# Performance work log

Hardware: AMD Instinct MI355X
Metric: run time of the kernel (lower is better)

Reference implementation:

```python
import jax, jax.numpy as jnp
import numpy as np


def conv2d(x, w, b):
    # x: [B,C,H,W], w: [O,C,K,K] (VALID, stride 1)
    out = jax.lax.conv_general_dilated(
        x, w, window_strides=(1, 1), padding='VALID',
        dimension_numbers=('NCHW', 'OIHW', 'NCHW'))
    return out + b[None, :, None, None]


def deform_conv2d(x, offset, w, b):
    # torchvision DeformConv2d semantics, offset_groups=1, stride=1, padding=0.
    # x: [B,C,H,W]; offset: [B, 2*K*K, Ho, Wo] with (dy, dx) interleaved per tap.
    B, C, H, W = x.shape
    O, _, K, _ = w.shape
    KK = K * K
    Ho, Wo = H - K + 1, W - K + 1
    off = offset.reshape(B, KK, 2, Ho, Wo)
    ky = (jnp.arange(KK) // K).astype(x.dtype)
    kx = (jnp.arange(KK) % K).astype(x.dtype)
    # sampling positions p0 + p_k + dp  -> [B, KK, Ho, Wo]
    py = ky[None, :, None, None] + jnp.arange(Ho, dtype=x.dtype)[None, None, :, None] + off[:, :, 0]
    px = kx[None, :, None, None] + jnp.arange(Wo, dtype=x.dtype)[None, None, None, :] + off[:, :, 1]
    y0 = jnp.floor(py)
    x0 = jnp.floor(px)
    wy = py - y0  # fractional parts
    wx = px - x0
    y0i = y0.astype(jnp.int32)
    x0i = x0.astype(jnp.int32)

    def corner(yi, xi):
        valid = ((yi >= 0) & (yi < H) & (xi >= 0) & (xi < W)).astype(x.dtype)
        yc = jnp.clip(yi, 0, H - 1)
        xc = jnp.clip(xi, 0, W - 1)
        # per-batch gather over all channels -> [B, C, KK, Ho, Wo]
        g = jax.vmap(lambda im, a, bb: im[:, a, bb])(x, yc, xc)
        return g * valid[:, None]

    v00 = corner(y0i, x0i)
    v01 = corner(y0i, x0i + 1)
    v10 = corner(y0i + 1, x0i)
    v11 = corner(y0i + 1, x0i + 1)
    wy_ = wy[:, None]  # [B,1,KK,Ho,Wo]
    wx_ = wx[:, None]
    samp = (v00 * (1 - wy_) * (1 - wx_) + v01 * (1 - wy_) * wx_
            + v10 * wy_ * (1 - wx_) + v11 * wy_ * wx_)
    out = jnp.einsum('bckhw,ock->bohw', samp, w.reshape(O, C, KK))
    return out + b[None, :, None, None]


_STAGES = [
    # (in_ch, out_ch, K)
    (1, 16, 3), (16, 32, 3), (32, 16, 5), (16, 16, 7), (16, 8, 5), (8, 4, 3),
]


def setup_inputs() -> dict:
    key = jax.random.key(0)
    keys = iter(jax.random.split(key, 64))
    inp = {'x': jax.random.normal(next(keys), (512, 1, 33, 33), dtype=jnp.float32)}
    for i, (ci, co, k) in enumerate(_STAGES, start=1):
        # offset-predicting conv: small init so offsets stay near the regular grid
        inp[f'ow{i}'] = jax.random.normal(next(keys), (2 * k * k, ci, k, k), dtype=jnp.float32) * 0.05
        inp[f'ob{i}'] = jax.random.normal(next(keys), (2 * k * k,), dtype=jnp.float32) * 0.05
        scale = 1.0 / np.sqrt(ci * k * k)
        inp[f'w{i}'] = jax.random.normal(next(keys), (co, ci, k, k), dtype=jnp.float32) * scale
        inp[f'b{i}'] = jax.random.normal(next(keys), (co,), dtype=jnp.float32) * scale
    inp['fc1_w'] = jax.random.normal(next(keys), (256, 13 * 13 * 4), dtype=jnp.float32) * (1.0 / np.sqrt(676))
    inp['fc1_b'] = jnp.zeros((256,), dtype=jnp.float32)
    inp['fc2_w'] = jax.random.normal(next(keys), (10, 256), dtype=jnp.float32) * (1.0 / np.sqrt(256))
    inp['fc2_b'] = jnp.zeros((10,), dtype=jnp.float32)
    return inp


def reference(x, ow1, ob1, w1, b1, ow2, ob2, w2, b2, ow3, ob3, w3, b3,
              ow4, ob4, w4, b4, ow5, ob5, w5, b5, ow6, ob6, w6, b6,
              fc1_w, fc1_b, fc2_w, fc2_b):
    h = jax.nn.relu(deform_conv2d(x, conv2d(x, ow1, ob1), w1, b1))
    h = jax.nn.relu(deform_conv2d(h, conv2d(h, ow2, ob2), w2, b2))
    h = deform_conv2d(h, conv2d(h, ow3, ob3), w3, b3)  # NOTE: no ReLU on stage 3 (matches source)
    h = jax.nn.relu(deform_conv2d(h, conv2d(h, ow4, ob4), w4, b4))
    h = jax.nn.relu(deform_conv2d(h, conv2d(h, ow5, ob5), w5, b5))
    h = jax.nn.relu(deform_conv2d(h, conv2d(h, ow6, ob6), w6, b6))
    flat = h.reshape(h.shape[0], -1)  # [B, 4*13*13]
    z = jax.nn.relu(flat @ fc1_w.T + fc1_b)
    return z @ fc2_w.T + fc2_b
```

## Files before the change

kernel.cpp:

```cpp
#include <hip/hip_runtime.h>

typedef __attribute__((ext_vector_type(8))) short bf16x8;
typedef __attribute__((ext_vector_type(4))) float f32x4;
typedef unsigned short ushort_t;

__device__ inline ushort_t bf16_trunc(float f) { return (ushort_t)(__float_as_uint(f) >> 16); }
__device__ inline float bf16_to_f(ushort_t u) { return __uint_as_float(((unsigned int)u) << 16); }

template<int CI, int KK, int KKPAD, int NPAD, int OC>
__global__ __launch_bounds__(256)
void wprep(const float* __restrict__ w, ushort_t* __restrict__ bhi, ushort_t* __restrict__ blo)
{
    const int idx = blockIdx.x * 256 + threadIdx.x;
    if (idx >= KKPAD * NPAD * CI) return;
    const int kk  = idx / (NPAD * CI);
    const int rem = idx - kk * (NPAD * CI);
    const int n   = rem / CI;
    const int ci  = rem - n * CI;
    const float v = (kk < KK && n < OC) ? w[((size_t)n * CI + ci) * KK + kk] : 0.f;
    const ushort_t h = bf16_trunc(v);
    bhi[idx] = h;
    blo[idx] = bf16_trunc(v - bf16_to_f(h));
}

template<int CI, int KK, int TPAD, int NPAD, int OC>
__global__ __launch_bounds__(256)
void wprep_d(const float* __restrict__ w, ushort_t* __restrict__ bhi, ushort_t* __restrict__ blo)
{
    constexpr int NPASS = (CI + 7) / 8;
    constexpr int TOTAL = NPASS * TPAD * NPAD * 8;
    const int idx = blockIdx.x * 256 + threadIdx.x;
    if (idx >= TOTAL) return;
    const int j     = idx & 7;
    const int n     = (idx >> 3) % NPAD;
    const int kslot = (idx >> 3) / NPAD;
    const int pass  = kslot / TPAD;
    const int tap   = kslot - pass * TPAD;
    const int ci    = pass * 8 + j;
    const float v = (tap < KK && n < OC && ci < CI) ? w[((size_t)n * CI + ci) * KK + tap] : 0.f;
    const ushort_t h = bf16_trunc(v);
    bhi[idx] = h;
    blo[idx] = bf16_trunc(v - bf16_to_f(h));
}

template<int CI, int K, int H, int W, int Ho, int Wo, int OC, int NTTOT, int NT0, int KSTEPS>
__global__ __launch_bounds__(256)
void conv_mfma(const ushort_t* __restrict__ Xhi, const ushort_t* __restrict__ Xlo,
               const ushort_t* __restrict__ Bhi, const ushort_t* __restrict__ Blo,
               const float* __restrict__ bias, float* __restrict__ out, int Mtotal)
{
    constexpr int NPAD = NTTOT * 16;
    constexpr int HW   = H * W;
    constexpr int HoWo = Ho * Wo;
    constexpr int NPASS = CI / 8;
    constexpr int TKS  = 32 / CI;
    constexpr int ROWS = TKS * NT0 * 16;
    constexpr int BSTR = CI + 8;
    constexpr int CH8  = CI / 8;
    constexpr int CHUNKS = ROWS * CH8;

    __shared__ __align__(16) ushort_t sBh[2][ROWS * BSTR];
    __shared__ __align__(16) ushort_t sBl[2][ROWS * BSTR];

    const int tid  = threadIdx.x;
    const int lane = tid & 63;
    const int wid  = tid >> 6;
    const int col  = lane & 15;
    const int quad = lane >> 4;

    const int mBase  = blockIdx.x * 256 + wid * 64;
    const int ntBase = blockIdx.y * NT0;

    int aBase[4];
#pragma unroll
    for (int mt = 0; mt < 4; ++mt) {
        int mm = mBase + mt * 16 + col;
        if (mm >= Mtotal) mm = Mtotal - 1;
        const int b   = mm / HoWo;
        const int pos = mm - b * HoWo;
        const int oy  = pos / Wo;
        const int ox  = pos - oy * Wo;
        aBase[mt] = b * NPASS * HW + oy * W + ox;
    }

    f32x4 acc[4][NT0];
#pragma unroll
    for (int mt = 0; mt < 4; ++mt)
#pragma unroll
        for (int nt = 0; nt < NT0; ++nt) acc[mt][nt] = (f32x4){0.f, 0.f, 0.f, 0.f};

    auto loadSlab = [&](int ks, int buf) {
        const int tap0 = ks * TKS;
        for (int i = tid; i < CHUNKS; i += 256) {
            const int row = i / CH8;
            const int c8  = i - row * CH8;
            const int t   = row / (NT0 * 16);
            const int nn  = row - t * (NT0 * 16);
            int n = ntBase * 16 + nn;
            if (n > NPAD - 1) n = NPAD - 1;
            const int g = ((tap0 + t) * NPAD + n) * CI + c8 * 8;
            *(bf16x8*)(sBh[buf] + row * BSTR + c8 * 8) = *(const bf16x8*)(Bhi + g);
            *(bf16x8*)(sBl[buf] + row * BSTR + c8 * 8) = *(const bf16x8*)(Blo + g);
        }
    };

    loadSlab(0, 0);
    __syncthreads();

#pragma unroll
    for (int ks = 0; ks < KSTEPS; ++ks) {
        if (ks + 1 < KSTEPS) loadSlab(ks + 1, (ks + 1) & 1);

        const int k0   = ks * 32 + quad * 8;
        const int tap  = k0 / CI;
        const int tloc = tap - ks * TKS;
        const int ci   = k0 - tap * CI;
        const int g    = ci >> 3;
        const int dkk  = (tap / K) * W + (tap - (tap / K) * K);

        bf16x8 ah[4], al[4];
#pragma unroll
        for (int mt = 0; mt < 4; ++mt) {
            const size_t aoff = (size_t)(aBase[mt] + g * HW + dkk) * 8;
            ah[mt] = *(const bf16x8*)(Xhi + aoff);
            al[mt] = *(const bf16x8*)(Xlo + aoff);
        }
        const ushort_t* __restrict__ bhp = sBh[ks & 1];
        const ushort_t* __restrict__ blp = sBl[ks & 1];
#pragma unroll
        for (int nt = 0; nt < NT0; ++nt) {
            const int ntg = ntBase + nt;
            if (ntg < NTTOT) {
                const int lrow = ((tloc * NT0 + nt) * 16 + col) * BSTR + ci;
                const bf16x8 bh = *(const bf16x8*)(bhp + lrow);
                const bf16x8 bl = *(const bf16x8*)(blp + lrow);
#pragma unroll
                for (int mt = 0; mt < 4; ++mt) {
                    acc[mt][nt] = __builtin_amdgcn_mfma_f32_16x16x32_bf16(ah[mt], bh, acc[mt][nt], 0, 0, 0);
                    acc[mt][nt] = __builtin_amdgcn_mfma_f32_16x16x32_bf16(al[mt], bh, acc[mt][nt], 0, 0, 0);
                    acc[mt][nt] = __builtin_amdgcn_mfma_f32_16x16x32_bf16(ah[mt], bl, acc[mt][nt], 0, 0, 0);
                }
            }
        }
        __syncthreads();
    }

#pragma unroll
    for (int mt = 0; mt < 4; ++mt) {
#pragma unroll
        for (int nt = 0; nt < NT0; ++nt) {
            const int ntg = ntBase + nt;
            const int n   = ntg * 16 + col;
            if (ntg < NTTOT && n < OC) {
                const float bv = bias[n];
#pragma unroll
                for (int r = 0; r < 4; ++r) {
                    const int m = mBase + mt * 16 + quad * 4 + r;
                    if (m < Mtotal) {
                        const int b   = m / HoWo;
                        const int pos = m - b * HoWo;
                        out[((size_t)b * OC + n) * HoWo + pos] = acc[mt][nt][r] + bv;
                    }
                }
            }
        }
    }
}

template<int K, int CI, int CO, int H, int W, int Ho, int Wo, bool RELU,
         int MT, int TPAD, bool OUTPL>
__global__ __launch_bounds__(MT * 64)
void deform_mfma(const ushort_t* __restrict__ Xhi, const ushort_t* __restrict__ Xlo,
                 const float* __restrict__ off,
                 const ushort_t* __restrict__ Bph, const ushort_t* __restrict__ Bpl,
                 const float* __restrict__ bias,
                 float* __restrict__ outF, ushort_t* __restrict__ oHi, ushort_t* __restrict__ oLo)
{
    constexpr int KK     = K * K;
    constexpr int HW     = H * W;
    constexpr int HoWo   = Ho * Wo;
    constexpr int NPASS  = CI / 8;
    constexpr int NPO    = CO / 8;
    constexpr int NT     = (CO + 15) / 16;
    constexpr int NPAD   = NT * 16;
    constexpr int STRIDE = 12;
    constexpr int nMB    = (HoWo + MT * 16 - 1) / (MT * 16);
    constexpr int THREADS = MT * 64;
    __shared__ __align__(16) float tile[HW * STRIDE];

    const int b    = blockIdx.x / nMB;
    const int mb   = blockIdx.x - b * nMB;
    const int tid  = threadIdx.x;
    const int wid  = tid >> 6;
    const int lane = tid & 63;
    const int col  = lane & 15;
    const int quad = lane >> 4;

    const int pixel0 = (mb * MT + wid) * 16;
    const int s      = pixel0 + col;
    const bool am    = (s < HoWo);
    const int oy = s / Wo, ox = s - oy * Wo;

    const float* offB = off + (size_t)b * 2 * KK * HoWo;

    f32x4 acc[NT];
#pragma unroll
    for (int nt = 0; nt < NT; ++nt) acc[nt] = (f32x4){0.f, 0.f, 0.f, 0.f};

    for (int pass = 0; pass < NPASS; ++pass) {
        __syncthreads();
        for (int pos = tid; pos < HW; pos += THREADS) {
            const size_t g = ((size_t)(b * NPASS + pass) * HW + pos) * 8;
            const bf16x8 h8 = *(const bf16x8*)(Xhi + g);
            const bf16x8 l8 = *(const bf16x8*)(Xlo + g);
#pragma unroll
            for (int c = 0; c < 8; ++c)
                tile[pos * STRIDE + c] = bf16_to_f((ushort_t)h8[c]) + bf16_to_f((ushort_t)l8[c]);
        }
        __syncthreads();

#pragma unroll
        for (int tg = 0; tg < TPAD / 4; ++tg) {
            const int tap = tg * 4 + quad;
            bf16x8 ahi = (bf16x8){0,0,0,0,0,0,0,0};
            bf16x8 alo = (bf16x8){0,0,0,0,0,0,0,0};

            if (am && tap < KK) {
                const float dy = offB[(size_t)(2 * tap + 0) * HoWo + s];
                const float dx = offB[(size_t)(2 * tap + 1) * HoWo + s];
                const float py = (float)(tap / K + oy) + dy;
                const float px = (float)(tap % K + ox) + dx;
                const float y0f = floorf(py), x0f = floorf(px);
                const float wy = py - y0f, wx = px - x0f;
                const int y0 = (int)y0f, x0 = (int)x0f;
                const int y1 = y0 + 1,   x1 = x0 + 1;

                const float m00 = (y0 >= 0 && y0 < H && x0 >= 0 && x0 < W) ? 1.f : 0.f;
                const float m01 = (y0 >= 0 && y0 < H && x1 >= 0 && x1 < W) ? 1.f : 0.f;
                const float m10 = (y1 >= 0 && y1 < H && x0 >= 0 && x0 < W) ? 1.f : 0.f;
                const float m11 = (y1 >= 0 && y1 < H && x1 >= 0 && x1 < W) ? 1.f : 0.f;

                const float w00 = (1.f - wy) * (1.f - wx) * m00;
                const float w01 = (1.f - wy) * wx         * m01;
                const float w10 = wy         * (1.f - wx) * m10;
                const float w11 = wy         * wx         * m11;

                const int y0c = min(max(y0, 0), H - 1), y1c = min(max(y1, 0), H - 1);
                const int x0c = min(max(x0, 0), W - 1), x1c = min(max(x1, 0), W - 1);
                const int i00 = (y0c * W + x0c) * STRIDE;
                const int i01 = (y0c * W + x1c) * STRIDE;
                const int i10 = (y1c * W + x0c) * STRIDE;
                const int i11 = (y1c * W + x1c) * STRIDE;

                float v00[8], v01[8], v10[8], v11[8];
                *(f32x4*)(v00) = *(const f32x4*)(tile + i00); *(f32x4*)(v00 + 4) = *(const f32x4*)(tile + i00 + 4);
                *(f32x4*)(v01) = *(const f32x4*)(tile + i01); *(f32x4*)(v01 + 4) = *(const f32x4*)(tile + i01 + 4);
                *(f32x4*)(v10) = *(const f32x4*)(tile + i10); *(f32x4*)(v10 + 4) = *(const f32x4*)(tile + i10 + 4);
                *(f32x4*)(v11) = *(const f32x4*)(tile + i11); *(f32x4*)(v11 + 4) = *(const f32x4*)(tile + i11 + 4);
#pragma unroll
                for (int j = 0; j < 8; ++j) {
                    const float sv = fmaf(v11[j], w11, fmaf(v10[j], w10,
                                     fmaf(v01[j], w01, v00[j] * w00)));
                    const ushort_t h = bf16_trunc(sv);
                    ahi[j] = (short)h;
                    alo[j] = (short)bf16_trunc(sv - bf16_to_f(h));
                }
            }

            const size_t kslot = (size_t)(pass * TPAD + tap);
#pragma unroll
            for (int nt = 0; nt < NT; ++nt) {
                const bf16x8 bh = *(const bf16x8*)(Bph + (kslot * NPAD + nt * 16 + col) * 8);
                const bf16x8 bl = *(const bf16x8*)(Bpl + (kslot * NPAD + nt * 16 + col) * 8);
                acc[nt] = __builtin_amdgcn_mfma_f32_16x16x32_bf16(ahi, bh, acc[nt], 0, 0, 0);
                acc[nt] = __builtin_amdgcn_mfma_f32_16x16x32_bf16(alo, bh, acc[nt], 0, 0, 0);
                acc[nt] = __builtin_amdgcn_mfma_f32_16x16x32_bf16(ahi, bl, acc[nt], 0, 0, 0);
            }
        }
    }

#pragma unroll
    for (int nt = 0; nt < NT; ++nt) {
        const int n = nt * 16 + col;
        if (n < CO) {
            const float bv = bias[n];
#pragma unroll
            for (int r = 0; r < 4; ++r) {
                const int m = pixel0 + quad * 4 + r;
                if (m < HoWo) {
                    float v = acc[nt][r] + bv;
                    if (RELU) v = fmaxf(v, 0.f);
                    if (OUTPL) {
                        const size_t o = (((size_t)b * NPO + (n >> 3)) * HoWo + m) * 8 + (n & 7);
                        const ushort_t h = bf16_trunc(v);
                        oHi[o] = h;
                        oLo[o] = bf16_trunc(v - bf16_to_f(h));
                    } else {
                        outF[((size_t)b * CO + n) * HoWo + m] = v;
                    }
                }
            }
        }
    }
}

template<int K, int CI, int CO, int H, int W, int Ho, int Wo, bool RELU,
         int CSPLIT, int STRIDE, int THREADS, int SPLIT, bool OUTPL>
__global__ __launch_bounds__(THREADS)
void deform_lds(const float* __restrict__ x, const float* __restrict__ off,
                const float* __restrict__ w, const float* __restrict__ bias,
                float* __restrict__ outF, ushort_t* __restrict__ oHi, ushort_t* __restrict__ oLo)
{
    constexpr int KK    = K * K;
    constexpr int HW    = H * W;
    constexpr int HoWo  = Ho * Wo;
    constexpr int NPASS = CI / CSPLIT;
    constexpr int NPO   = (CO + 7) / 8;
    constexpr int CHUNK = (HoWo + SPLIT - 1) / SPLIT;
    static_assert(CHUNK <= THREADS, "chunk must fit in one block");
    __shared__ __align__(16) float tile[HW * STRIDE];

    const int b   = blockIdx.x / SPLIT;
    const int sp  = blockIdx.x - b * SPLIT;
    const int tid = threadIdx.x;
    const int s   = sp * CHUNK + tid;
    const bool active = (tid < CHUNK) && (s < HoWo);

    const int oy = s / Wo, ox = s - oy * Wo;
    const float* offp = off + ((size_t)b * 2 * KK) * HoWo + s;

    float acc[CO];
#pragma unroll
    for (int o = 0; o < CO; ++o) acc[o] = 0.f;

    for (int pass = 0; pass < NPASS; ++pass) {
        const int cbase = pass * CSPLIT;
        __syncthreads();
        for (int pos = tid; pos < HW; pos += THREADS) {
#pragma unroll
            for (int c = 0; c < CSPLIT; ++c)
                tile[pos * STRIDE + c] = x[((size_t)b * CI + (cbase + c)) * HW + pos];
        }
        __syncthreads();

        if (active) {
            for (int kk = 0; kk < KK; ++kk) {
                const float dy = offp[(size_t)(2 * kk + 0) * HoWo];
                const float dx = offp[(size_t)(2 * kk + 1) * HoWo];
                const float py = (float)(kk / K + oy) + dy;
                const float px = (float)(kk % K + ox) + dx;
                const float y0f = floorf(py), x0f = floorf(px);
                const float wy = py - y0f, wx = px - x0f;
                const int y0 = (int)y0f, x0 = (int)x0f;
                const int y1 = y0 + 1,   x1 = x0 + 1;

                const float m00 = (y0 >= 0 && y0 < H && x0 >= 0 && x0 < W) ? 1.f : 0.f;
                const float m01 = (y0 >= 0 && y0 < H && x1 >= 0 && x1 < W) ? 1.f : 0.f;
                const float m10 = (y1 >= 0 && y1 < H && x0 >= 0 && x0 < W) ? 1.f : 0.f;
                const float m11 = (y1 >= 0 && y1 < H && x1 >= 0 && x1 < W) ? 1.f : 0.f;

                const float w00 = (1.f - wy) * (1.f - wx) * m00;
                const float w01 = (1.f - wy) * wx         * m01;
                const float w10 = wy         * (1.f - wx) * m10;
                const float w11 = wy         * wx         * m11;

                const int y0c = min(max(y0, 0), H - 1), y1c = min(max(y1, 0), H - 1);
                const int x0c = min(max(x0, 0), W - 1), x1c = min(max(x1, 0), W - 1);
                const int i00 = (y0c * W + x0c) * STRIDE;
                const int i01 = (y0c * W + x1c) * STRIDE;
                const int i10 = (y1c * W + x0c) * STRIDE;
                const int i11 = (y1c * W + x1c) * STRIDE;

                if constexpr (CSPLIT % 4 == 0) {
#pragma unroll
                    for (int cg = 0; cg < CSPLIT; cg += 4) {
                        const f32x4 v00 = *(const f32x4*)(tile + i00 + cg);
                        const f32x4 v01 = *(const f32x4*)(tile + i01 + cg);
                        const f32x4 v10 = *(const f32x4*)(tile + i10 + cg);
                        const f32x4 v11 = *(const f32x4*)(tile + i11 + cg);
#pragma unroll
                        for (int j = 0; j < 4; ++j) {
                            const float sv = fmaf(v11[j], w11, fmaf(v10[j], w10,
                                             fmaf(v01[j], w01, v00[j] * w00)));
#pragma unroll
                            for (int o = 0; o < CO; ++o)
                                acc[o] = fmaf(sv, w[(size_t)(o * CI + cbase + cg + j) * KK + kk], acc[o]);
                        }
                    }
                } else {
                    const float sv = fmaf(tile[i11], w11, fmaf(tile[i10], w10,
                                     fmaf(tile[i01], w01, tile[i00] * w00)));
#pragma unroll
                    for (int o = 0; o < CO; ++o)
                        acc[o] = fmaf(sv, w[(size_t)(o * CI + cbase) * KK + kk], acc[o]);
                }
            }
        }
    }

    if (active) {
#pragma unroll
        for (int o = 0; o < CO; ++o) {
            float v = acc[o] + bias[o];
            if (RELU) v = fmaxf(v, 0.f);
            if (OUTPL) {
                const size_t oi = (((size_t)b * NPO + (o >> 3)) * HoWo + s) * 8 + (o & 7);
                const ushort_t h = bf16_trunc(v);
                oHi[oi] = h;
                oLo[oi] = bf16_trunc(v - bf16_to_f(h));
            } else {
                outF[((size_t)b * CO + o) * HoWo + s] = v;
            }
        }
    }
}

template<int K, int CI, int NOC, int OC, int H, int W, int Ho, int Wo, int PIX>
__global__ __launch_bounds__(256)
void conv_tile(const float* __restrict__ x, const float* __restrict__ w,
               const float* __restrict__ bias, float* __restrict__ out)
{
    constexpr int KK   = K * K;
    constexpr int HoWo = Ho * Wo;
    constexpr int WoG  = (Wo + PIX - 1) / PIX;
    constexpr int G    = Ho * WoG;
    constexpr int XV   = PIX + K - 1;

    const int oc0   = blockIdx.y * NOC;
    const int g_all = blockIdx.x * 256 + threadIdx.x;
    const int b     = g_all / G;
    const int g     = g_all - b * G;
    const int oy    = g / WoG;
    const int ox0   = (g - oy * WoG) * PIX;

    const float* xbp = x + (b * CI) * (H * W) + oy * W + ox0;
    const float* wp  = w + oc0 * (CI * KK);

    float acc[PIX][NOC];
#pragma unroll
    for (int p = 0; p < PIX; ++p)
#pragma unroll
        for (int j = 0; j < NOC; ++j) acc[p][j] = bias[oc0 + j];

    const int lim = W - 1 - ox0;

    for (int ci = 0; ci < CI; ++ci) {
        const float* xc = xbp + ci * (H * W);
#pragma unroll
        for (int ky = 0; ky < K; ++ky) {
            float xv[XV];
#pragma unroll
            for (int i = 0; i < XV; ++i) {
                const int off = (i <= lim) ? i : lim;
                xv[i] = xc[ky * W + off];
            }
#pragma unroll
            for (int kx = 0; kx < K; ++kx) {
#pragma unroll
                for (int p = 0; p < PIX; ++p) {
                    const float v = xv[p + kx];
#pragma unroll
                    for (int j = 0; j < NOC; ++j)
                        acc[p][j] = fmaf(v, wp[j * (CI * KK) + ci * KK + ky * K + kx], acc[p][j]);
                }
            }
        }
    }

    float* op = out + (b * OC + oc0) * HoWo + oy * Wo + ox0;
#pragma unroll
    for (int p = 0; p < PIX; ++p) {
        if (ox0 + p < Wo) {
#pragma unroll
            for (int j = 0; j < NOC; ++j) op[j * HoWo + p] = acc[p][j];
        }
    }
}

template<int IN, int OUT>
__global__ __launch_bounds__(256)
void wtrans(const float* __restrict__ w, float* __restrict__ wt)
{
    const int idx = blockIdx.x * 256 + threadIdx.x;
    if (idx >= IN * OUT) return;
    const int i = idx / OUT, j = idx - i * OUT;
    wt[idx] = w[(size_t)j * IN + i];
}

template<int IN, int OUT, bool RELU>
__global__ __launch_bounds__(256)
void fc_t(const float* __restrict__ h, const float* __restrict__ wt,
          const float* __restrict__ bias, float* __restrict__ out, int B)
{
    const int idx = blockIdx.x * 256 + threadIdx.x;
    if (idx >= B * OUT) return;
    const int b = idx / OUT;
    const int j = idx - b * OUT;
    const float* hb = h + (size_t)b * IN;
    float acc = bias[j];
#pragma unroll 4
    for (int i = 0; i < IN; ++i)
        acc = fmaf(hb[i], wt[(size_t)i * OUT + j], acc);
    if (RELU) acc = fmaxf(acc, 0.f);
    out[idx] = acc;
}

extern "C" void kernel_launch(void* const* d_in, const int* in_sizes, int n_in,
                              void* d_out, int out_size, void* d_ws, size_t ws_size,
                              hipStream_t stream)
{
    const int B = 512;
    const float* x = (const float*)d_in[0];
    const float *ow[6], *ob[6], *w[6], *bi[6];
    for (int i = 0; i < 6; ++i) {
        ow[i] = (const float*)d_in[1 + 4 * i];
        ob[i] = (const float*)d_in[2 + 4 * i];
        w[i]  = (const float*)d_in[3 + 4 * i];
        bi[i] = (const float*)d_in[4 + 4 * i];
    }
    const float* fc1w = (const float*)d_in[25];
    const float* fc1b = (const float*)d_in[26];
    const float* fc2w = (const float*)d_in[27];
    const float* fc2b = (const float*)d_in[28];
    float* out = (float*)d_out;

    float* P   = (float*)d_ws;
    float* Q   = P  + 14000000;
    float* OFF = Q  + 14000000;
    float* Z   = OFF + 18200000;
    ushort_t* WBhi = (ushort_t*)(Z + 200000);
    ushort_t* WBlo = WBhi + 200000;
    ushort_t* WDhi = WBlo + 200000;
    ushort_t* WDlo = WDhi + 200000;
    float* WT1 = (float*)(WDlo + 200000);
    float* WT2 = WT1 + 173056;

    const dim3 blk(256);
    #define GRIDT(Ho, Wo, PIX, NG) dim3((B * (Ho) * (((Wo) + (PIX) - 1) / (PIX)) + 255) / 256, (NG), 1)
    #define CEILDIV(a, b) (((a) + (b) - 1) / (b))

    ushort_t* PL2h = (ushort_t*)Q;  ushort_t* PL2l = PL2h + (size_t)(B * 961 + 2048) * 16;
    ushort_t* PL3h = (ushort_t*)P;  ushort_t* PL3l = PL3h + (size_t)(B * 841 + 2048) * 32;
    ushort_t* PL4h = (ushort_t*)Q;  ushort_t* PL4l = PL4h + (size_t)(B * 625 + 2048) * 16;
    ushort_t* PL5h = (ushort_t*)P;  ushort_t* PL5l = PL5h + (size_t)(B * 361 + 2048) * 16;

    conv_tile<3, 1, 6, 18, 33, 33, 31, 31, 4><<<GRIDT(31, 31, 4, 3), blk, 0, stream>>>(x, ow[0], ob[0], OFF);
    deform_lds<3, 1, 16, 33, 33, 31, 31, true, 1, 1, 512, 2, true><<<dim3(B * 2), dim3(512), 0, stream>>>(x, OFF, w[0], bi[0], nullptr, PL2h, PL2l);

    {
        const int Mv = B * 841;
        wprep<16, 9, 10, 32, 18><<<CEILDIV(10 * 32 * 16, 256), blk, 0, stream>>>(ow[1], WBhi, WBlo);
        conv_mfma<16, 3, 31, 31, 29, 29, 18, 2, 2, 5><<<dim3(CEILDIV(Mv, 256), 1), blk, 0, stream>>>(PL2h, PL2l, WBhi, WBlo, ob[1], OFF, Mv);
        wprep_d<16, 9, 12, 32, 32><<<CEILDIV(2 * 12 * 32 * 8, 256), blk, 0, stream>>>(w[1], WDhi, WDlo);
        deform_mfma<3, 16, 32, 31, 31, 29, 29, true, 8, 12, true><<<dim3(B * 7), dim3(512), 0, stream>>>(PL2h, PL2l, OFF, WDhi, WDlo, bi[1], nullptr, PL3h, PL3l);
    }
    {
        const int Mv = B * 625;
        wprep<32, 25, 25, 64, 50><<<CEILDIV(25 * 64 * 32, 256), blk, 0, stream>>>(ow[2], WBhi, WBlo);
        conv_mfma<32, 5, 29, 29, 25, 25, 50, 4, 4, 25><<<dim3(CEILDIV(Mv, 256), 1), blk, 0, stream>>>(PL3h, PL3l, WBhi, WBlo, ob[2], OFF, Mv);
        wprep_d<32, 25, 28, 16, 16><<<CEILDIV(4 * 28 * 16 * 8, 256), blk, 0, stream>>>(w[2], WDhi, WDlo);
        deform_mfma<5, 32, 16, 29, 29, 25, 25, false, 8, 28, true><<<dim3(B * 5), dim3(512), 0, stream>>>(PL3h, PL3l, OFF, WDhi, WDlo, bi[2], nullptr, PL4h, PL4l);
    }
    {
        const int Mv = B * 361;
        wprep<16, 49, 50, 112, 98><<<CEILDIV(50 * 112 * 16, 256), blk, 0, stream>>>(ow[3], WBhi, WBlo);
        conv_mfma<16, 7, 25, 25, 19, 19, 98, 7, 4, 25><<<dim3(CEILDIV(Mv, 256), 2), blk, 0, stream>>>(PL4h, PL4l, WBhi, WBlo, ob[3], OFF, Mv);
        wprep_d<16, 49, 52, 16, 16><<<CEILDIV(2 * 52 * 16 * 8, 256), blk, 0, stream>>>(w[3], WDhi, WDlo);
        deform_mfma<7, 16, 16, 25, 25, 19, 19, true, 8, 52, true><<<dim3(B * 3), dim3(512), 0, stream>>>(PL4h, PL4l, OFF, WDhi, WDlo, bi[3], nullptr, PL5h, PL5l);
    }
    {
        const int Mv = B * 225;
        wprep<16, 25, 26, 64, 50><<<CEILDIV(26 * 64 * 16, 256), blk, 0, stream>>>(ow[4], WBhi, WBlo);
        conv_mfma<16, 5, 19, 19, 15, 15, 50, 4, 4, 13><<<dim3(CEILDIV(Mv, 256), 1), blk, 0, stream>>>(PL5h, PL5l, WBhi, WBlo, ob[4], OFF, Mv);
        wprep_d<16, 25, 28, 16, 8><<<CEILDIV(2 * 28 * 16 * 8, 256), blk, 0, stream>>>(w[4], WDhi, WDlo);
        deform_mfma<5, 16, 8, 19, 19, 15, 15, true, 4, 28, false><<<dim3(B * 4), dim3(256), 0, stream>>>(PL5h, PL5l, OFF, WDhi, WDlo, bi[4], Q, nullptr, nullptr);
    }
    conv_tile<3, 8, 6, 18, 15, 15, 13, 13, 4><<<GRIDT(13, 13, 4, 3), blk, 0, stream>>>(Q, ow[5], ob[5], OFF);
    deform_lds<3, 8, 4, 15, 15, 13, 13, true, 8, 12, 192, 1, false><<<dim3(B), dim3(192), 0, stream>>>(Q, OFF, w[5], bi[5], P, nullptr, nullptr);

    wtrans<676, 256><<<CEILDIV(676 * 256, 256), blk, 0, stream>>>(fc1w, WT1);
    wtrans<256, 10><<<CEILDIV(256 * 10, 256), blk, 0, stream>>>(fc2w, WT2);
    fc_t<676, 256, true><<<dim3(CEILDIV(B * 256, 256)), blk, 0, stream>>>(P, WT1, fc1b, Z, B);
    fc_t<256, 10, false><<<dim3(CEILDIV(B * 10, 256)), blk, 0, stream>>>(Z, WT2, fc2b, out, B);

    #undef GRIDT
    #undef CEILDIV
}
```

Before: 902.4 us.

## Stage 16 channels per pass and reuse bilinear weights across passes

The deformable-conv MFMA kernel now stages 16 channels per LDS pass instead of 8, which halves the number of barrier-separated passes. Bilinear weights and corner indices are computed once in the first pass and kept in registers for later passes, so offset loads and sampling-coordinate math are not repeated. The hi/lo bf16 split is vectorised with byte-permute instructions, and launch bounds now request 4 waves per EU. In exchange, the LDS tile per block is larger and the per-tap arrays add register pressure, which may reduce occupancy or cause spills. The new static_assert requires CI to be a multiple of 16.

```diff
diff --git a/kernel.cpp b/kernel.cpp
--- a/kernel.cpp
+++ b/kernel.cpp
@@ -2,10 +2,35 @@
 
 typedef __attribute__((ext_vector_type(8))) short bf16x8;
 typedef __attribute__((ext_vector_type(4))) float f32x4;
+typedef __attribute__((ext_vector_type(4))) unsigned int u32x4;
 typedef unsigned short ushort_t;
 
 __device__ inline ushort_t bf16_trunc(float f) { return (ushort_t)(__float_as_uint(f) >> 16); }
 __device__ inline float bf16_to_f(ushort_t u) { return __uint_as_float(((unsigned int)u) << 16); }
+
+__device__ inline unsigned int hi_pair(unsigned int u1, unsigned int u0) {
+    return __builtin_amdgcn_perm(u1, u0, 0x07060302u);
+}
+
+__device__ inline void split8(const f32x4 sA, const f32x4 sB, bf16x8& ahi, bf16x8& alo)
+{
+    unsigned int u[8], h[8], d[8];
+#pragma unroll
+    for (int j = 0; j < 4; ++j) {
+        u[j]     = __float_as_uint(sA[j]);
+        u[4 + j] = __float_as_uint(sB[j]);
+    }
+#pragma unroll
+    for (int j = 0; j < 8; ++j) {
+        h[j] = u[j] & 0xffff0000u;
+        d[j] = __float_as_uint(__uint_as_float(u[j]) - __uint_as_float(h[j]));
+    }
+    union { u32x4 w; bf16x8 v; } H, L;
+    H.w = (u32x4){hi_pair(h[1], h[0]), hi_pair(h[3], h[2]), hi_pair(h[5], h[4]), hi_pair(h[7], h[6])};
+    L.w = (u32x4){hi_pair(d[1], d[0]), hi_pair(d[3], d[2]), hi_pair(d[5], d[4]), hi_pair(d[7], d[6])};
+    ahi = H.v;
+    alo = L.v;
+}
 
 template<int CI, int KK, int KKPAD, int NPAD, int OC>
 __global__ __launch_bounds__(256)
@@ -169,24 +194,27 @@
 
 template<int K, int CI, int CO, int H, int W, int Ho, int Wo, bool RELU,
          int MT, int TPAD, bool OUTPL>
-__global__ __launch_bounds__(MT * 64)
+__global__ __launch_bounds__(MT * 64, 4)
 void deform_mfma(const ushort_t* __restrict__ Xhi, const ushort_t* __restrict__ Xlo,
                  const float* __restrict__ off,
                  const ushort_t* __restrict__ Bph, const ushort_t* __restrict__ Bpl,
                  const float* __restrict__ bias,
                  float* __restrict__ outF, ushort_t* __restrict__ oHi, ushort_t* __restrict__ oLo)
 {
+    static_assert(CI % 16 == 0, "deform_mfma v2 stages 16 channels per pass");
     constexpr int KK     = K * K;
     constexpr int HW     = H * W;
     constexpr int HoWo   = Ho * Wo;
-    constexpr int NPASS  = CI / 8;
+    constexpr int NG8    = CI / 8;
+    constexpr int NPASS  = CI / 16;
     constexpr int NPO    = CO / 8;
     constexpr int NT     = (CO + 15) / 16;
     constexpr int NPAD   = NT * 16;
-    constexpr int STRIDE = 12;
+    constexpr int TSTR   = 20;
+    constexpr int TG     = TPAD / 4;
     constexpr int nMB    = (HoWo + MT * 16 - 1) / (MT * 16);
     constexpr int THREADS = MT * 64;
-    __shared__ __align__(16) float tile[HW * STRIDE];
+    __shared__ __align__(16) float tile[HW * TSTR];
 
     const int b    = blockIdx.x / nMB;
     const int mb   = blockIdx.x - b * nMB;
@@ -207,74 +235,112 @@
 #pragma unroll
     for (int nt = 0; nt < NT; ++nt) acc[nt] = (f32x4){0.f, 0.f, 0.f, 0.f};
 
+    float pw00[TG], pw01[TG], pw10[TG], pw11[TG];
+    int   pi00[TG], pi01[TG], pi10[TG], pi11[TG];
+    if constexpr (NPASS > 1) {
+#pragma unroll
+        for (int t = 0; t < TG; ++t) {
+            pw00[t] = pw01[t] = pw10[t] = pw11[t] = 0.f;
+            pi00[t] = pi01[t] = pi10[t] = pi11[t] = 0;
+        }
+    }
+
+#pragma unroll
     for (int pass = 0; pass < NPASS; ++pass) {
         __syncthreads();
         for (int pos = tid; pos < HW; pos += THREADS) {
-            const size_t g = ((size_t)(b * NPASS + pass) * HW + pos) * 8;
-            const bf16x8 h8 = *(const bf16x8*)(Xhi + g);
-            const bf16x8 l8 = *(const bf16x8*)(Xlo + g);
-#pragma unroll
-            for (int c = 0; c < 8; ++c)
-                tile[pos * STRIDE + c] = bf16_to_f((ushort_t)h8[c]) + bf16_to_f((ushort_t)l8[c]);
+            const size_t gbase = ((size_t)(b * NG8 + pass * 2) * HW + pos) * 8;
+            const bf16x8 h0 = *(const bf16x8*)(Xhi + gbase);
+            const bf16x8 l0 = *(const bf16x8*)(Xlo + gbase);
+            const bf16x8 h1 = *(const bf16x8*)(Xhi + gbase + (size_t)HW * 8);
+            const bf16x8 l1 = *(const bf16x8*)(Xlo + gbase + (size_t)HW * 8);
+            f32x4 v0, v1, v2, v3;
+#pragma unroll
+            for (int j = 0; j < 4; ++j) {
+                v0[j] = bf16_to_f((ushort_t)h0[j])     + bf16_to_f((ushort_t)l0[j]);
+                v1[j] = bf16_to_f((ushort_t)h0[4 + j]) + bf16_to_f((ushort_t)l0[4 + j]);
+                v2[j] = bf16_to_f((ushort_t)h1[j])     + bf16_to_f((ushort_t)l1[j]);
+                v3[j] = bf16_to_f((ushort_t)h1[4 + j]) + bf16_to_f((ushort_t)l1[4 + j]);
+            }
+            float* tp = tile + pos * TSTR;
+            *(f32x4*)(tp + 0)  = v0;
+            *(f32x4*)(tp + 4)  = v1;
+            *(f32x4*)(tp + 8)  = v2;
+            *(f32x4*)(tp + 12) = v3;
         }
         __syncthreads();
 
 #pragma unroll
-        for (int tg = 0; tg < TPAD / 4; ++tg) {
+        for (int tg = 0; tg < TG; ++tg) {
             const int tap = tg * 4 + quad;
-            bf16x8 ahi = (bf16x8){0,0,0,0,0,0,0,0};
-            bf16x8 alo = (bf16x8){0,0,0,0,0,0,0,0};
-
-            if (am && tap < KK) {
-                const float dy = offB[(size_t)(2 * tap + 0) * HoWo + s];
-                const float dx = offB[(size_t)(2 * tap + 1) * HoWo + s];
-                const float py = (float)(tap / K + oy) + dy;
-                const float px = (float)(tap % K + ox) + dx;
-                const float y0f = floorf(py), x0f = floorf(px);
-                const float wy = py - y0f, wx = px - x0f;
-                const int y0 = (int)y0f, x0 = (int)x0f;
-                const int y1 = y0 + 1,   x1 = x0 + 1;
-
-                const float m00 = (y0 >= 0 && y0 < H && x0 >= 0 && x0 < W) ? 1.f : 0.f;
-                const float m01 = (y0 >= 0 && y0 < H && x1 >= 0 && x1 < W) ? 1.f : 0.f;
-                const float m10 = (y1 >= 0 && y1 < H && x0 >= 0 && x0 < W) ? 1.f : 0.f;
-                const float m11 = (y1 >= 0 && y1 < H && x1 >= 0 && x1 < W) ? 1.f : 0.f;
-
-                const float w00 = (1.f - wy) * (1.f - wx) * m00;
-                const float w01 = (1.f - wy) * wx         * m01;
-                const float w10 = wy         * (1.f - wx) * m10;
-                const float w11 = wy         * wx         * m11;
-
-                const int y0c = min(max(y0, 0), H - 1), y1c = min(max(y1, 0), H - 1);
-                const int x0c = min(max(x0, 0), W - 1), x1c = min(max(x1, 0), W - 1);
-                const int i00 = (y0c * W + x0c) * STRIDE;
-                const int i01 = (y0c * W + x1c) * STRIDE;
-                const int i10 = (y1c * W + x0c) * STRIDE;
-                const int i11 = (y1c * W + x1c) * STRIDE;
-
-                float v00[8], v01[8], v10[8], v11[8];
-                *(f32x4*)(v00) = *(const f32x4*)(tile + i00); *(f32x4*)(v00 + 4) = *(const f32x4*)(tile + i00 + 4);
-                *(f32x4*)(v01) = *(const f32x4*)(tile + i01); *(f32x4*)(v01 + 4) = *(const f32x4*)(tile + i01 + 4);
-                *(f32x4*)(v10) = *(const f32x4*)(tile + i10); *(f32x4*)(v10 + 4) = *(const f32x4*)(tile + i10 + 4);
-                *(f32x4*)(v11) = *(const f32x4*)(tile + i11); *(f32x4*)(v11 + 4) = *(const f32x4*)(tile + i11 + 4);
-#pragma unroll
-                for (int j = 0; j < 8; ++j) {
-                    const float sv = fmaf(v11[j], w11, fmaf(v10[j], w10,
-                                     fmaf(v01[j], w01, v00[j] * w00)));
-                    const ushort_t h = bf16_trunc(sv);
-                    ahi[j] = (short)h;
-                    alo[j] = (short)bf16_trunc(sv - bf16_to_f(h));
-                }
-            }
-
-            const size_t kslot = (size_t)(pass * TPAD + tap);
-#pragma unroll
-            for (int nt = 0; nt < NT; ++nt) {
-                const bf16x8 bh = *(const bf16x8*)(Bph + (kslot * NPAD + nt * 16 + col) * 8);
-                const bf16x8 bl = *(const bf16x8*)(Bpl + (kslot * NPAD + nt * 16 + col) * 8);
-                acc[nt] = __builtin_amdgcn_mfma_f32_16x16x32_bf16(ahi, bh, acc[nt], 0, 0, 0);
-                acc[nt] = __builtin_amdgcn_mfma_f32_16x16x32_bf16(alo, bh, acc[nt], 0, 0, 0);
-                acc[nt] = __builtin_amdgcn_mfma_f32_16x16x32_bf16(ahi, bl, acc[nt], 0, 0, 0);
+
+            float w00 = 0.f, w01 = 0.f, w10 = 0.f, w11 = 0.f;
+            int   i00 = 0,   i01 = 0,   i10 = 0,   i11 = 0;
+
+            if (pass == 0) {
+                if (am && tap < KK) {
+                    const float dy = offB[(size_t)(2 * tap + 0) * HoWo + s];
+                    const float dx = offB[(size_t)(2 * tap + 1) * HoWo + s];
+                    const float py = (float)(tap / K + oy) + dy;
+                    const float px = (float)(tap % K + ox) + dx;
+                    const float y0f = floorf(py), x0f = floorf(px);
+                    const float wy = py - y0f, wx = px - x0f;
+                    const int y0 = (int)y0f, x0 = (int)x0f;
+                    const int y1 = y0 + 1,   x1 = x0 + 1;
+
+                    const float m00 = (y0 >= 0 && y0 < H && x0 >= 0 && x0 < W) ? 1.f : 0.f;
+                    const float m01 = (y0 >= 0 && y0 < H && x1 >= 0 && x1 < W) ? 1.f : 0.f;
+                    const float m10 = (y1 >= 0 && y1 < H && x0 >= 0 && x0 < W) ? 1.f : 0.f;
+                    const float m11 = (y1 >= 0 && y1 < H && x1 >= 0 && x1 < W) ? 1.f : 0.f;
+
+                    w00 = (1.f - wy) * (1.f - wx) * m00;
+                    w01 = (1.f - wy) * wx         * m01;
+                    w10 = wy         * (1.f - wx) * m10;
+                    w11 = wy         * wx         * m11;
+
+                    const int y0c = min(max(y0, 0), H - 1), y1c = min(max(y1, 0), H - 1);
+                    const int x0c = min(max(x0, 0), W - 1), x1c = min(max(x1, 0), W - 1);
+                    i00 = (y0c * W + x0c) * TSTR;
+                    i01 = (y0c * W + x1c) * TSTR;
+                    i10 = (y1c * W + x0c) * TSTR;
+                    i11 = (y1c * W + x1c) * TSTR;
+                }
+                if constexpr (NPASS > 1) {
+                    pw00[tg] = w00; pw01[tg] = w01; pw10[tg] = w10; pw11[tg] = w11;
+                    pi00[tg] = i00; pi01[tg] = i01; pi10[tg] = i10; pi11[tg] = i11;
+                }
+            } else if constexpr (NPASS > 1) {
+                w00 = pw00[tg]; w01 = pw01[tg]; w10 = pw10[tg]; w11 = pw11[tg];
+                i00 = pi00[tg]; i01 = pi01[tg]; i10 = pi10[tg]; i11 = pi11[tg];
+            }
+
+#pragma unroll
+            for (int g = 0; g < 2; ++g) {
+                const float* tp = tile + g * 8;
+                const f32x4 a00 = *(const f32x4*)(tp + i00);
+                const f32x4 c00 = *(const f32x4*)(tp + i00 + 4);
+                const f32x4 a01 = *(const f32x4*)(tp + i01);
+                const f32x4 c01 = *(const f32x4*)(tp + i01 + 4);
+                const f32x4 a10 = *(const f32x4*)(tp + i10);
+                const f32x4 c10 = *(const f32x4*)(tp + i10 + 4);
+                const f32x4 a11 = *(const f32x4*)(tp + i11);
+                const f32x4 c11 = *(const f32x4*)(tp + i11 + 4);
+
+                f32x4 sA = a00 * w00 + a01 * w01 + a10 * w10 + a11 * w11;
+                f32x4 sB = c00 * w00 + c01 * w01 + c10 * w10 + c11 * w11;
+
+                bf16x8 ahi, alo;
+                split8(sA, sB, ahi, alo);
+
+                const int kslot = (pass * 2 + g) * TPAD + tap;
+#pragma unroll
+                for (int nt = 0; nt < NT; ++nt) {
+                    const bf16x8 bh = *(const bf16x8*)(Bph + ((size_t)kslot * NPAD + nt * 16 + col) * 8);
+                    const bf16x8 bl = *(const bf16x8*)(Bpl + ((size_t)kslot * NPAD + nt * 16 + col) * 8);
+                    acc[nt] = __builtin_amdgcn_mfma_f32_16x16x32_bf16(ahi, bh, acc[nt], 0, 0, 0);
+                    acc[nt] = __builtin_amdgcn_mfma_f32_16x16x32_bf16(alo, bh, acc[nt], 0, 0, 0);
+                    acc[nt] = __builtin_amdgcn_mfma_f32_16x16x32_bf16(ahi, bl, acc[nt], 0, 0, 0);
+                }
             }
         }
     }
```

New measurement: 866.8 us. 1.04x faster.
